# Optimization experiments

Measured on AMD Instinct MI355X. Metric: run time of the kernel, lower is better.

The kernel has to match this reference:

```python
import jax, jax.numpy as jnp
import numpy as np


def setup_inputs() -> dict:
    key = jax.random.key(0)
    kq, kk, kv = jax.random.split(key, 3)
    B, S, D = 16, 2048, 128
    q = jax.random.normal(kq, (B, S, D), dtype=jnp.float32)
    k = jax.random.normal(kk, (B, S, D), dtype=jnp.float32)
    v = jax.random.normal(kv, (B, S, D), dtype=jnp.float32)
    return {"q": q, "k": k, "v": v}


def reference(q, k, v):
    # scores = q @ k^T * scale  (scale = 1/sqrt(head_dim), the standard value
    # passed to this module; dropout=0.0 and attn_mask=None per defaults)
    scale = q.shape[-1] ** -0.5
    scores = jnp.einsum('bqd,bkd->bqk', q, k) * scale  # [B, S, S]
    attention = jax.nn.softmax(scores, axis=-1)
    context = jnp.einsum('bqk,bkd->bqd', attention, v)  # [B, S, D]
    return (context, attention)
```

## Files before the change

kernel.cpp:

```cpp
#include <hip/hip_runtime.h>

#define SS 2048
#define DD 128
#define NB 16
#define TM 64
#define TN 64
#define NITER (SS / TN)

typedef short bf16x8 __attribute__((ext_vector_type(8)));
typedef float f32x4 __attribute__((ext_vector_type(4)));

#define KSTRIDE 136
#define VSTRIDE 72
#define PSTRIDE 72

#define SL2E (0.08838834764831845f * 1.4426950408889634f)

__device__ __forceinline__ unsigned short f2bf(float x) {
    unsigned u = __builtin_bit_cast(unsigned, x);
    u += 0x7fffu + ((u >> 16) & 1u);
    return (unsigned short)(u >> 16);
}

__device__ __forceinline__ float fexp2(float x) {
#if __has_builtin(__builtin_amdgcn_exp2f)
    return __builtin_amdgcn_exp2f(x);
#else
    return __expf(x * 0.6931471805599453f);
#endif
}

__global__ void prep_kernel(const float* __restrict__ k, const float* __restrict__ v,
                            unsigned short* __restrict__ kb, unsigned short* __restrict__ vt) {
    __shared__ unsigned short t[64 * 72];
    const int x = blockIdx.x, b = blockIdx.z, sb = blockIdx.y * 64;
    const int tid = threadIdx.x;
    if (x < 2) {
        const int db = x * 64;
        const int r16 = tid >> 4, c4 = (tid & 15) * 4;
        for (int i = 0; i < 4; ++i) {
            int sl = i * 16 + r16;
            float4 xx = *(const float4*)(v + ((size_t)(b * SS + sb + sl) * DD + db + c4));
            ushort4 u; u.x = f2bf(xx.x); u.y = f2bf(xx.y); u.z = f2bf(xx.z); u.w = f2bf(xx.w);
            *(ushort4*)&t[sl * 72 + c4] = u;
        }
        __syncthreads();
        for (int i = 0; i < 4; ++i) {
            int dl = i * 16 + r16;
            ushort4 u;
            u.x = t[(c4 + 0) * 72 + dl];
            u.y = t[(c4 + 1) * 72 + dl];
            u.z = t[(c4 + 2) * 72 + dl];
            u.w = t[(c4 + 3) * 72 + dl];
            *(ushort4*)(vt + ((size_t)(b * DD + db + dl) * SS + sb + c4)) = u;
        }
    } else {
        const int c0 = (x - 2) * 64;
        for (int i = 0; i < 4; ++i) {
            int e = i * 1024 + tid * 4;
            int r = e >> 6, c = e & 63;
            size_t off = (size_t)(b * SS + sb + r) * DD + c0 + c;
            float4 xx = *(const float4*)(k + off);
            ushort4 u; u.x = f2bf(xx.x); u.y = f2bf(xx.y); u.z = f2bf(xx.z); u.w = f2bf(xx.w);
            *(ushort4*)(kb + off) = u;
        }
    }
}

__global__ __launch_bounds__(512, 4)
void attn_kernel(const float* __restrict__ q,
                 const unsigned short* __restrict__ kb,
                 const unsigned short* __restrict__ vt,
                 float* __restrict__ attn, float* __restrict__ ctx) {
    __shared__ unsigned short K_lds[TN * KSTRIDE];
    __shared__ unsigned short V_lds[DD * VSTRIDE];
    __shared__ unsigned short P_lds[TM * PSTRIDE];
    __shared__ float rs_lds[TM];
    __shared__ float inv_lds[TM];

    const int tid = threadIdx.x;
    const int lane = tid & 63, w = tid >> 6;
    const int wm = w >> 2, wn = w & 3;
    const int l15 = lane & 15, quad = lane >> 4;

    const int bid = blockIdx.x;
    const int bb = ((bid & 7) << 1) | ((bid >> 3) & 1);
    const int q0 = (bid >> 4) * TM;

    if (tid < TM) rs_lds[tid] = 0.0f;

    bf16x8 qf[2][4];
    {
        const float* qg = q + ((size_t)(bb * SS + q0 + wm * 32 + l15)) * DD + quad * 8;
        for (int mi = 0; mi < 2; ++mi)
            for (int kk = 0; kk < 4; ++kk) {
                float4 a = *(const float4*)(qg + mi * 16 * DD + kk * 32);
                float4 b = *(const float4*)(qg + mi * 16 * DD + kk * 32 + 4);
                bf16x8 f;
                f[0] = (short)f2bf(a.x); f[1] = (short)f2bf(a.y);
                f[2] = (short)f2bf(a.z); f[3] = (short)f2bf(a.w);
                f[4] = (short)f2bf(b.x); f[5] = (short)f2bf(b.y);
                f[6] = (short)f2bf(b.z); f[7] = (short)f2bf(b.w);
                qf[mi][kk] = f;
            }
    }

    const unsigned short* kgb = kb + (size_t)bb * SS * DD;
    const unsigned short* vgb = vt + (size_t)bb * DD * SS;

    float rs[8];
    for (int j = 0; j < 8; ++j) rs[j] = 0.0f;

    for (int it = 0; it < NITER; ++it) {
        __syncthreads();
        {
            const unsigned short* kg = kgb + (size_t)(it * TN) * DD;
            for (int c = 0; c < 2; ++c) {
                int e = c * 4096 + tid * 8;
                *(bf16x8*)&K_lds[(e >> 7) * KSTRIDE + (e & 127)] = *(const bf16x8*)(kg + e);
            }
        }
        __syncthreads();
        f32x4 acc[2];
        acc[0] = (f32x4){0.f, 0.f, 0.f, 0.f};
        acc[1] = (f32x4){0.f, 0.f, 0.f, 0.f};
        for (int kk = 0; kk < 4; ++kk) {
            bf16x8 bfv = *(const bf16x8*)&K_lds[(wn * 16 + l15) * KSTRIDE + kk * 32 + quad * 8];
            for (int mi = 0; mi < 2; ++mi)
                acc[mi] = __builtin_amdgcn_mfma_f32_16x16x32_bf16(qf[mi][kk], bfv, acc[mi], 0, 0, 0);
        }
        for (int mi = 0; mi < 2; ++mi)
            for (int r = 0; r < 4; ++r)
                rs[mi * 4 + r] += fexp2(acc[mi][r] * SL2E);
    }

    for (int j = 0; j < 8; ++j) {
        float s = rs[j];
        s += __shfl_xor(s, 1, 64);
        s += __shfl_xor(s, 2, 64);
        s += __shfl_xor(s, 4, 64);
        s += __shfl_xor(s, 8, 64);
        rs[j] = s;
    }
    if (l15 == 0)
        for (int mi = 0; mi < 2; ++mi)
            for (int r = 0; r < 4; ++r)
                atomicAdd(&rs_lds[wm * 32 + mi * 16 + quad * 4 + r], rs[mi * 4 + r]);
    __syncthreads();
    if (tid < TM) inv_lds[tid] = 1.0f / rs_lds[tid];
    __syncthreads();
    float inv[8];
    for (int mi = 0; mi < 2; ++mi)
        for (int r = 0; r < 4; ++r)
            inv[mi * 4 + r] = inv_lds[wm * 32 + mi * 16 + quad * 4 + r];

    f32x4 cacc[2][2];
    for (int mi = 0; mi < 2; ++mi)
        for (int ni = 0; ni < 2; ++ni) cacc[mi][ni] = (f32x4){0.f, 0.f, 0.f, 0.f};

    float* ap[8];
    for (int mi = 0; mi < 2; ++mi)
        for (int r = 0; r < 4; ++r)
            ap[mi * 4 + r] = attn + (size_t)bb * SS * SS
                           + (size_t)(q0 + wm * 32 + mi * 16 + quad * 4 + r) * SS
                           + wn * 16 + l15;

    for (int it = 0; it < NITER; ++it) {
        const int k0 = it * TN;
        __syncthreads();
        {
            const unsigned short* kg = kgb + (size_t)k0 * DD;
            for (int c = 0; c < 2; ++c) {
                int e = c * 4096 + tid * 8;
                *(bf16x8*)&K_lds[(e >> 7) * KSTRIDE + (e & 127)] = *(const bf16x8*)(kg + e);
            }
            const unsigned short* vg = vgb + k0;
            for (int c = 0; c < 2; ++c) {
                int e = c * 4096 + tid * 8;
                int dr = e >> 6, ck = e & 63;
                *(bf16x8*)&V_lds[dr * VSTRIDE + ck] = *(const bf16x8*)(vg + (size_t)dr * SS + ck);
            }
        }
        __syncthreads();

        f32x4 acc[2];
        acc[0] = (f32x4){0.f, 0.f, 0.f, 0.f};
        acc[1] = (f32x4){0.f, 0.f, 0.f, 0.f};
        for (int kk = 0; kk < 4; ++kk) {
            bf16x8 bfv = *(const bf16x8*)&K_lds[(wn * 16 + l15) * KSTRIDE + kk * 32 + quad * 8];
            for (int mi = 0; mi < 2; ++mi)
                acc[mi] = __builtin_amdgcn_mfma_f32_16x16x32_bf16(qf[mi][kk], bfv, acc[mi], 0, 0, 0);
        }

        for (int mi = 0; mi < 2; ++mi)
            for (int r = 0; r < 4; ++r) {
                float p = fexp2(acc[mi][r] * SL2E) * inv[mi * 4 + r];
                ap[mi * 4 + r][0] = p;
                P_lds[(wm * 32 + mi * 16 + quad * 4 + r) * PSTRIDE + wn * 16 + l15] = f2bf(p);
            }
        for (int j = 0; j < 8; ++j) ap[j] += TN;
        __syncthreads();

        for (int kk = 0; kk < 2; ++kk) {
            bf16x8 af[2];
            for (int mi = 0; mi < 2; ++mi)
                af[mi] = *(const bf16x8*)&P_lds[(wm * 32 + mi * 16 + l15) * PSTRIDE + kk * 32 + quad * 8];
            for (int ni = 0; ni < 2; ++ni) {
                bf16x8 bv = *(const bf16x8*)&V_lds[(wn * 32 + ni * 16 + l15) * VSTRIDE + kk * 32 + quad * 8];
                for (int mi = 0; mi < 2; ++mi)
                    cacc[mi][ni] = __builtin_amdgcn_mfma_f32_16x16x32_bf16(af[mi], bv, cacc[mi][ni], 0, 0, 0);
            }
        }
    }

    float* cg = ctx + ((size_t)(bb * SS) + q0) * DD;
    for (int mi = 0; mi < 2; ++mi)
        for (int ni = 0; ni < 2; ++ni)
            for (int r = 0; r < 4; ++r) {
                int row = wm * 32 + mi * 16 + quad * 4 + r;
                int col = wn * 32 + ni * 16 + l15;
                cg[(size_t)row * DD + col] = cacc[mi][ni][r];
            }
}

extern "C" void kernel_launch(void* const* d_in, const int* in_sizes, int n_in,
                              void* d_out, int out_size, void* d_ws, size_t ws_size,
                              hipStream_t stream) {
    const float* q = (const float*)d_in[0];
    const float* k = (const float*)d_in[1];
    const float* v = (const float*)d_in[2];
    float* ctx = (float*)d_out;
    float* attn = ctx + (size_t)NB * SS * DD;

    unsigned short* kb = (unsigned short*)d_ws;
    unsigned short* vt = kb + (size_t)NB * SS * DD;

    prep_kernel<<<dim3(4, SS / 64, NB), 256, 0, stream>>>(k, v, kb, vt);
    attn_kernel<<<dim3((SS / TM) * NB), 512, 0, stream>>>(q, kb, vt, attn, ctx);
}
```

Before: 374.1 us.

## Load K/V fragments directly from global, double-buffer P, drop LDS staging barriers

Removes the K and V shared-memory staging in both passes. Each wave now reads its MFMA operand fragments straight from global memory (L2-resident bf16), and the next K tile is prefetched into registers. P is double-buffered in LDS, so each iteration needs only one barrier instead of three. The change also adds s_setprio around the MFMA blocks and nontemporal stores for the attention and context outputs. The cost is redundant global loads across waves that share fragments, in exchange for fewer syncs and less LDS traffic.

```diff
diff --git a/kernel.cpp b/kernel.cpp
--- a/kernel.cpp
+++ b/kernel.cpp
@@ -10,8 +10,6 @@
 typedef short bf16x8 __attribute__((ext_vector_type(8)));
 typedef float f32x4 __attribute__((ext_vector_type(4)));
 
-#define KSTRIDE 136
-#define VSTRIDE 72
 #define PSTRIDE 72
 
 #define SL2E (0.08838834764831845f * 1.4426950408889634f)
@@ -29,6 +27,9 @@
     return __expf(x * 0.6931471805599453f);
 #endif
 }
+
+#define LGKM0() asm volatile("s_waitcnt lgkmcnt(0)" ::: "memory")
+#define BAR()   __builtin_amdgcn_s_barrier()
 
 __global__ void prep_kernel(const float* __restrict__ k, const float* __restrict__ v,
                             unsigned short* __restrict__ kb, unsigned short* __restrict__ vt) {
@@ -72,9 +73,7 @@
                  const unsigned short* __restrict__ kb,
                  const unsigned short* __restrict__ vt,
                  float* __restrict__ attn, float* __restrict__ ctx) {
-    __shared__ unsigned short K_lds[TN * KSTRIDE];
-    __shared__ unsigned short V_lds[DD * VSTRIDE];
-    __shared__ unsigned short P_lds[TM * PSTRIDE];
+    __shared__ unsigned short P_lds[2][TM * PSTRIDE];
     __shared__ float rs_lds[TM];
     __shared__ float inv_lds[TM];
 
@@ -110,30 +109,28 @@
 
     float rs[8];
     for (int j = 0; j < 8; ++j) rs[j] = 0.0f;
-
-    for (int it = 0; it < NITER; ++it) {
-        __syncthreads();
-        {
-            const unsigned short* kg = kgb + (size_t)(it * TN) * DD;
-            for (int c = 0; c < 2; ++c) {
-                int e = c * 4096 + tid * 8;
-                *(bf16x8*)&K_lds[(e >> 7) * KSTRIDE + (e & 127)] = *(const bf16x8*)(kg + e);
-            }
-        }
-        __syncthreads();
-        f32x4 acc[2];
-        acc[0] = (f32x4){0.f, 0.f, 0.f, 0.f};
-        acc[1] = (f32x4){0.f, 0.f, 0.f, 0.f};
-        for (int kk = 0; kk < 4; ++kk) {
-            bf16x8 bfv = *(const bf16x8*)&K_lds[(wn * 16 + l15) * KSTRIDE + kk * 32 + quad * 8];
-            for (int mi = 0; mi < 2; ++mi)
-                acc[mi] = __builtin_amdgcn_mfma_f32_16x16x32_bf16(qf[mi][kk], bfv, acc[mi], 0, 0, 0);
-        }
-        for (int mi = 0; mi < 2; ++mi)
-            for (int r = 0; r < 4; ++r)
-                rs[mi * 4 + r] += fexp2(acc[mi][r] * SL2E);
-    }
-
+    {
+        const unsigned short* kp = kgb + (size_t)(wn * 16 + l15) * DD + quad * 8;
+#pragma unroll 2
+        for (int it = 0; it < NITER; ++it) {
+            f32x4 a0 = (f32x4){0.f, 0.f, 0.f, 0.f};
+            f32x4 a1 = (f32x4){0.f, 0.f, 0.f, 0.f};
+#pragma unroll
+            for (int kk = 0; kk < 4; ++kk) {
+                bf16x8 kf = *(const bf16x8*)(kp + kk * 32);
+                a0 = __builtin_amdgcn_mfma_f32_16x16x32_bf16(qf[0][kk], kf, a0, 0, 0, 0);
+                a1 = __builtin_amdgcn_mfma_f32_16x16x32_bf16(qf[1][kk], kf, a1, 0, 0, 0);
+            }
+#pragma unroll
+            for (int r = 0; r < 4; ++r) {
+                rs[r]     += fexp2(a0[r] * SL2E);
+                rs[4 + r] += fexp2(a1[r] * SL2E);
+            }
+            kp += TN * DD;
+        }
+    }
+
+#pragma unroll
     for (int j = 0; j < 8; ++j) {
         float s = rs[j];
         s += __shfl_xor(s, 1, 64);
@@ -142,6 +139,7 @@
         s += __shfl_xor(s, 8, 64);
         rs[j] = s;
     }
+    __syncthreads();
     if (l15 == 0)
         for (int mi = 0; mi < 2; ++mi)
             for (int r = 0; r < 4; ++r)
@@ -149,77 +147,88 @@
     __syncthreads();
     if (tid < TM) inv_lds[tid] = 1.0f / rs_lds[tid];
     __syncthreads();
-    float inv[8];
+    float inv[2][4];
     for (int mi = 0; mi < 2; ++mi)
         for (int r = 0; r < 4; ++r)
-            inv[mi * 4 + r] = inv_lds[wm * 32 + mi * 16 + quad * 4 + r];
+            inv[mi][r] = inv_lds[wm * 32 + mi * 16 + quad * 4 + r];
 
     f32x4 cacc[2][2];
     for (int mi = 0; mi < 2; ++mi)
         for (int ni = 0; ni < 2; ++ni) cacc[mi][ni] = (f32x4){0.f, 0.f, 0.f, 0.f};
 
-    float* ap[8];
-    for (int mi = 0; mi < 2; ++mi)
-        for (int r = 0; r < 4; ++r)
-            ap[mi * 4 + r] = attn + (size_t)bb * SS * SS
-                           + (size_t)(q0 + wm * 32 + mi * 16 + quad * 4 + r) * SS
-                           + wn * 16 + l15;
+    float* ab = attn + (size_t)bb * SS * SS
+              + (size_t)(q0 + wm * 32) * SS + (wn * 16 + l15);
+    const unsigned short* kp0 = kgb + (size_t)(wn * 16 + l15) * DD + quad * 8;
+    const unsigned short* vfp = vgb + (size_t)(wn * 32 + l15) * SS + quad * 8;
+
+    bf16x8 kf[4];
+#pragma unroll
+    for (int kk = 0; kk < 4; ++kk) kf[kk] = *(const bf16x8*)(kp0 + kk * 32);
+    const unsigned short* kpn = kp0 + (size_t)TN * DD;
 
     for (int it = 0; it < NITER; ++it) {
         const int k0 = it * TN;
-        __syncthreads();
-        {
-            const unsigned short* kg = kgb + (size_t)k0 * DD;
-            for (int c = 0; c < 2; ++c) {
-                int e = c * 4096 + tid * 8;
-                *(bf16x8*)&K_lds[(e >> 7) * KSTRIDE + (e & 127)] = *(const bf16x8*)(kg + e);
-            }
-            const unsigned short* vg = vgb + k0;
-            for (int c = 0; c < 2; ++c) {
-                int e = c * 4096 + tid * 8;
-                int dr = e >> 6, ck = e & 63;
-                *(bf16x8*)&V_lds[dr * VSTRIDE + ck] = *(const bf16x8*)(vg + (size_t)dr * SS + ck);
-            }
-        }
-        __syncthreads();
 
         f32x4 acc[2];
         acc[0] = (f32x4){0.f, 0.f, 0.f, 0.f};
         acc[1] = (f32x4){0.f, 0.f, 0.f, 0.f};
+        __builtin_amdgcn_s_setprio(1);
+#pragma unroll
         for (int kk = 0; kk < 4; ++kk) {
-            bf16x8 bfv = *(const bf16x8*)&K_lds[(wn * 16 + l15) * KSTRIDE + kk * 32 + quad * 8];
-            for (int mi = 0; mi < 2; ++mi)
-                acc[mi] = __builtin_amdgcn_mfma_f32_16x16x32_bf16(qf[mi][kk], bfv, acc[mi], 0, 0, 0);
-        }
-
+            acc[0] = __builtin_amdgcn_mfma_f32_16x16x32_bf16(qf[0][kk], kf[kk], acc[0], 0, 0, 0);
+            acc[1] = __builtin_amdgcn_mfma_f32_16x16x32_bf16(qf[1][kk], kf[kk], acc[1], 0, 0, 0);
+        }
+        __builtin_amdgcn_s_setprio(0);
+
+        if (it < NITER - 1) {
+#pragma unroll
+            for (int kk = 0; kk < 4; ++kk) kf[kk] = *(const bf16x8*)(kpn + kk * 32);
+            kpn += (size_t)TN * DD;
+        }
+
+        bf16x8 bv[2][2];
+#pragma unroll
+        for (int kk = 0; kk < 2; ++kk)
+#pragma unroll
+            for (int ni = 0; ni < 2; ++ni)
+                bv[kk][ni] = *(const bf16x8*)(vfp + (size_t)(ni * 16) * SS + k0 + kk * 32);
+
+        unsigned short* pw = &P_lds[it & 1][0];
+#pragma unroll
         for (int mi = 0; mi < 2; ++mi)
+#pragma unroll
             for (int r = 0; r < 4; ++r) {
-                float p = fexp2(acc[mi][r] * SL2E) * inv[mi * 4 + r];
-                ap[mi * 4 + r][0] = p;
-                P_lds[(wm * 32 + mi * 16 + quad * 4 + r) * PSTRIDE + wn * 16 + l15] = f2bf(p);
-            }
-        for (int j = 0; j < 8; ++j) ap[j] += TN;
-        __syncthreads();
-
+                float p = fexp2(acc[mi][r] * SL2E) * inv[mi][r];
+                __builtin_nontemporal_store(p, ab + (size_t)((mi * 16 + quad * 4 + r) * SS) + k0);
+                pw[(wm * 32 + mi * 16 + quad * 4 + r) * PSTRIDE + wn * 16 + l15] = f2bf(p);
+            }
+
+        LGKM0();
+        BAR();
+
+        __builtin_amdgcn_s_setprio(1);
+#pragma unroll
         for (int kk = 0; kk < 2; ++kk) {
-            bf16x8 af[2];
-            for (int mi = 0; mi < 2; ++mi)
-                af[mi] = *(const bf16x8*)&P_lds[(wm * 32 + mi * 16 + l15) * PSTRIDE + kk * 32 + quad * 8];
-            for (int ni = 0; ni < 2; ++ni) {
-                bf16x8 bv = *(const bf16x8*)&V_lds[(wn * 32 + ni * 16 + l15) * VSTRIDE + kk * 32 + quad * 8];
-                for (int mi = 0; mi < 2; ++mi)
-                    cacc[mi][ni] = __builtin_amdgcn_mfma_f32_16x16x32_bf16(af[mi], bv, cacc[mi][ni], 0, 0, 0);
-            }
-        }
+            bf16x8 af0 = *(const bf16x8*)&pw[(wm * 32 +  0 + l15) * PSTRIDE + kk * 32 + quad * 8];
+            bf16x8 af1 = *(const bf16x8*)&pw[(wm * 32 + 16 + l15) * PSTRIDE + kk * 32 + quad * 8];
+            cacc[0][0] = __builtin_amdgcn_mfma_f32_16x16x32_bf16(af0, bv[kk][0], cacc[0][0], 0, 0, 0);
+            cacc[1][0] = __builtin_amdgcn_mfma_f32_16x16x32_bf16(af1, bv[kk][0], cacc[1][0], 0, 0, 0);
+            cacc[0][1] = __builtin_amdgcn_mfma_f32_16x16x32_bf16(af0, bv[kk][1], cacc[0][1], 0, 0, 0);
+            cacc[1][1] = __builtin_amdgcn_mfma_f32_16x16x32_bf16(af1, bv[kk][1], cacc[1][1], 0, 0, 0);
+        }
+        __builtin_amdgcn_s_setprio(0);
     }
 
     float* cg = ctx + ((size_t)(bb * SS) + q0) * DD;
+#pragma unroll
     for (int mi = 0; mi < 2; ++mi)
+#pragma unroll
         for (int ni = 0; ni < 2; ++ni)
+#pragma unroll
             for (int r = 0; r < 4; ++r) {
                 int row = wm * 32 + mi * 16 + quad * 4 + r;
                 int col = wn * 32 + ni * 16 + l15;
-                cg[(size_t)row * DD + col] = cacc[mi][ni][r];
+                __builtin_nontemporal_store(cacc[mi][ni][r], cg + (size_t)row * DD + col);
             }
 }
 
```

After: 455.2 us. +21.7%, slower.
